# Kernel tuning notes

Hardware: AMD Instinct MI355X
Metric: run time of the kernel (lower is better)

Reference implementation:

```python
import jax, jax.numpy as jnp
import numpy as np


def setup_inputs() -> dict:
    key = jax.random.key(0)
    k1, k2 = jax.random.split(key)
    n_nodes, n_feat, n_edges = 100000, 64, 1600000
    x = jax.random.normal(k1, (n_nodes, n_feat), dtype=jnp.float32)
    edge_index = jax.random.randint(k2, (2, n_edges), 0, n_nodes, dtype=jnp.int64)
    return {"x": x, "edge_index": edge_index}


def reference(x, edge_index):
    # Faithful JAX version of OneHopGCNNormNodeLabelAggregator.forward:
    #   adj = SparseTensor.from_edge_index(edge_index)  (values = 1)
    #   adj_norm = gcn_norm(adj)  -> add self-loops (diag=1), symmetric D^-1/2 A D^-1/2
    #   x_neighbors = adj_norm.t() @ x
    n = x.shape[0]
    self_loops = jnp.arange(n, dtype=edge_index.dtype)
    row = jnp.concatenate([edge_index[0], self_loops])  # source of adj entry A[row, col]
    col = jnp.concatenate([edge_index[1], self_loops])
    # degree over rows (sparsesum dim=1 after fill_diag)
    deg = jax.ops.segment_sum(jnp.ones(row.shape, x.dtype), row, num_segments=n)
    deg_inv_sqrt = jnp.where(deg > 0, jax.lax.rsqrt(deg), 0.0).astype(x.dtype)
    # symmetric norm weight per edge
    w = deg_inv_sqrt[row] * deg_inv_sqrt[col]  # [E+n]
    # adj_norm.t() @ x : out[col] += w * x[row]
    x_neighbors = jax.ops.segment_sum(w[:, None] * x[row], col, num_segments=n)
    return x_neighbors
```

## Files before the change

kernel.cpp:

```cpp
#include <hip/hip_runtime.h>

#define NFEAT 64
#define BSHIFT 8
#define BCOLS 256
#define NBMAX 512
#define CAP 5120
#define CHUNK 3136
#define NITP 7
#define TPB 512
#define FBIT (CAP / TPB)
#define QCAP 1664


__device__ __forceinline__ unsigned short f2bf(float f) {
    unsigned int u = __float_as_uint(f);
    return (unsigned short)((u + 0x7FFFu + ((u >> 16) & 1u)) >> 16);
}
__device__ __forceinline__ float bflo(unsigned int u) {
    return __uint_as_float(u << 16);
}
__device__ __forceinline__ float bfhi(unsigned int u) {
    return __uint_as_float(u & 0xFFFF0000u);
}

__device__ __forceinline__ int wave_incl_scan(int v, int lane) {
    #pragma unroll
    for (int off = 1; off < 64; off <<= 1) {
        int u = __shfl_up(v, off);
        if (lane >= off) v += u;
    }
    return v;
}

__global__ __launch_bounds__(TPB)
void k_partCR(const int* __restrict__ rows, const int* __restrict__ cols,
              int* __restrict__ bcur, int* __restrict__ bcurR,
              int* __restrict__ part, unsigned char* __restrict__ partR, int E) {
    __shared__ int histC[NBMAX];
    __shared__ int histR[NBMAX];
    __shared__ int gbaseC[NBMAX];
    __shared__ int gbaseR[NBMAX];
    __shared__ int wsumC[8];
    __shared__ int wsumR[8];
    __shared__ int stageC[CHUNK];
    __shared__ unsigned char stageR[CHUNK];
    __shared__ unsigned short bidC[CHUNK];
    __shared__ unsigned short bidR[CHUNK];
    int chunk0 = blockIdx.x * CHUNK;
    int cnt = min(CHUNK, E - chunk0);
    int t = threadIdx.x;
    int lane = t & 63, wid = t >> 6;

    histC[t] = 0; histR[t] = 0;
    __syncthreads();

    int pk[NITP];
    unsigned char rpk[NITP];
    unsigned short cb[NITP], rb[NITP];
    unsigned short rkC[NITP], rkR[NITP];
    #pragma unroll
    for (int k = 0; k < NITP; k++) {
        int i = t + k * TPB;
        if (i < cnt) {
            int c = cols[chunk0 + i];
            int r = rows[chunk0 + i];
            int b  = c >> BSHIFT;
            int b2 = r >> BSHIFT;
            pk[k]  = ((c & (BCOLS - 1)) << 17) | r;
            rpk[k] = (unsigned char)(r & (BCOLS - 1));
            cb[k] = (unsigned short)b;
            rb[k] = (unsigned short)b2;
            rkC[k] = (unsigned short)atomicAdd(&histC[b], 1);
            rkR[k] = (unsigned short)atomicAdd(&histR[b2], 1);
        }
    }
    __syncthreads();

    int v1 = histC[t];
    int inc1 = wave_incl_scan(v1, lane);
    if (lane == 63) wsumC[wid] = inc1;
    int v2 = histR[t];
    int inc2 = wave_incl_scan(v2, lane);
    if (lane == 63) wsumR[wid] = inc2;
    __syncthreads();
    int addC = 0, addR = 0;
    #pragma unroll
    for (int k = 0; k < 8; k++) {
        if (k < wid) { addC += wsumC[k]; addR += wsumR[k]; }
    }
    int exC = inc1 - v1 + addC;
    int exR = inc2 - v2 + addR;
    gbaseC[t] = (v1 > 0) ? (t * CAP + atomicAdd(&bcur[t],  v1) - exC) : 0;
    gbaseR[t] = (v2 > 0) ? (t * CAP + atomicAdd(&bcurR[t], v2) - exR) : 0;
    histC[t] = exC;
    histR[t] = exR;
    __syncthreads();

    #pragma unroll
    for (int k = 0; k < NITP; k++) {
        int i = t + k * TPB;
        if (i < cnt) {
            int p = histC[cb[k]] + rkC[k];
            stageC[p] = pk[k];
            bidC[p] = cb[k];
            int p2 = histR[rb[k]] + rkR[k];
            stageR[p2] = rpk[k];
            bidR[p2] = rb[k];
        }
    }
    __syncthreads();

    for (int p = t; p < cnt; p += TPB) {
        int b = bidC[p];
        int idx = gbaseC[b] + p;
        if (idx < (b + 1) * CAP) part[idx] = stageC[p];
        int b2 = bidR[p];
        int idx2 = gbaseR[b2] + p;
        if (idx2 < (b2 + 1) * CAP) partR[idx2] = stageR[p];
    }
}

__global__ __launch_bounds__(TPB)
void k_fillR(const unsigned char* __restrict__ partR, const int* __restrict__ bcurR,
             const float4* __restrict__ x4, float* __restrict__ dinv,
             unsigned short* __restrict__ xs, int n) {
    __shared__ int lcnt[64];
    __shared__ float ldinv[64];
    int qb = blockIdx.x;
    int b = qb >> 2, q = qb & 3;
    int s = b * CAP;
    int t = threadIdx.x;
    int cntR = min(bcurR[b], CAP);
    if (t < 64) lcnt[t] = 0;
    __syncthreads();
    int c4 = cntR >> 2;
    const uchar4* p4 = (const uchar4*)(partR + s);
    for (int i = t; i < c4; i += TPB) {
        uchar4 kk = p4[i];
        if ((kk.x >> 6) == q) atomicAdd(&lcnt[kk.x & 63], 1);
        if ((kk.y >> 6) == q) atomicAdd(&lcnt[kk.y & 63], 1);
        if ((kk.z >> 6) == q) atomicAdd(&lcnt[kk.z & 63], 1);
        if ((kk.w >> 6) == q) atomicAdd(&lcnt[kk.w & 63], 1);
    }
    for (int i = (c4 << 2) + t; i < cntR; i += TPB) {
        int key = partR[s + i];
        if ((key >> 6) == q) atomicAdd(&lcnt[key & 63], 1);
    }
    __syncthreads();
    int rows_base = (b << BSHIFT) + (q << 6);
    if (t < 64) {
        float d = rsqrtf((float)(lcnt[t] + 1));
        ldinv[t] = d;
        int gr = rows_base + t;
        if (gr < n) dinv[gr] = d;
    }
    __syncthreads();
    int nr = n - rows_base;
    if (nr <= 0) return;
    size_t base4 = (size_t)rows_base << 4;
    int lim = min(64, nr) << 4;
    for (int i = t; i < lim; i += TPB) {
        float dd = ldinv[i >> 4];
        float4 vv = x4[base4 + i];
        ushort4 o;
        o.x = f2bf(dd * vv.x); o.y = f2bf(dd * vv.y);
        o.z = f2bf(dd * vv.z); o.w = f2bf(dd * vv.w);
        ((ushort4*)xs)[base4 + i] = o;
    }
}

#define XSLD(r) (*((const uint4*)(xs + ((size_t)(r) << 6)) + li))
#define ACC8(u) { a0 += bflo(u.x); a1 += bfhi(u.x); \
                  a2 += bflo(u.y); a3 += bfhi(u.y); \
                  a4 += bflo(u.z); a5 += bfhi(u.z); \
                  a6 += bflo(u.w); a7 += bfhi(u.w); }

__global__ __launch_bounds__(TPB)
void k_fuse(const int* __restrict__ part, const int* __restrict__ bcur,
            const unsigned short* __restrict__ xs,
            const float* __restrict__ dinv,
            float4* __restrict__ out4, int n) {
    __shared__ int lcnt[64];
    __shared__ int lps[64];
    __shared__ int stage[QCAP];
    int qb = blockIdx.x;
    int b = qb >> 2, q = qb & 3;
    int s = b * CAP;
    int cnt = min(bcur[b], CAP);
    int t = threadIdx.x;

    if (t < 64) lcnt[t] = 0;
    __syncthreads();

    int pk[FBIT];
    short rk[FBIT];
    #pragma unroll
    for (int k = 0; k < FBIT; k++) {
        int i = t + k * TPB;
        int v2 = (i < cnt) ? part[s + i] : -1;
        pk[k] = v2;
        rk[k] = -1;
        if (v2 >= 0) {
            int c = v2 >> 17;
            if ((c >> 6) == q)
                rk[k] = (short)atomicAdd(&lcnt[c & 63], 1);
        }
    }
    __syncthreads();

    if (t < 64) {
        int v = lcnt[t];
        int inc = wave_incl_scan(v, t);
        lps[t] = inc - v;
    }
    __syncthreads();

    #pragma unroll
    for (int k = 0; k < FBIT; k++) {
        if (rk[k] >= 0) {
            int c = (pk[k] >> 17) & 63;
            int p = lps[c] + rk[k];
            if (p < QCAP) stage[p] = pk[k] & 0x1FFFF;
        }
    }
    __syncthreads();

    int g = t >> 3, li = t & 7;
    int node = (b << BSHIFT) + (q << 6) + g;
    if (node >= n) return;
    int ss = lps[g];
    int len = lcnt[g];
    if (ss + len > QCAP) len = QCAP > ss ? QCAP - ss : 0;
    float a0 = 0.f, a1 = 0.f, a2 = 0.f, a3 = 0.f;
    float a4 = 0.f, a5 = 0.f, a6 = 0.f, a7 = 0.f;
    int len4 = len & ~3;
    uint4 c0, c1, c2, c3;
    if (len4 > 0) {
        int r0 = stage[ss], r1 = stage[ss + 1];
        int r2 = stage[ss + 2], r3 = stage[ss + 3];
        c0 = XSLD(r0); c1 = XSLD(r1); c2 = XSLD(r2); c3 = XSLD(r3);
    }
    for (int i = 4; i < len4; i += 4) {
        int r0 = stage[ss + i],     r1 = stage[ss + i + 1];
        int r2 = stage[ss + i + 2], r3 = stage[ss + i + 3];
        uint4 n0 = XSLD(r0), n1 = XSLD(r1), n2 = XSLD(r2), n3 = XSLD(r3);
        ACC8(c0); ACC8(c1); ACC8(c2); ACC8(c3);
        c0 = n0; c1 = n1; c2 = n2; c3 = n3;
    }
    if (len4 > 0) { ACC8(c0); ACC8(c1); ACC8(c2); ACC8(c3); }
    for (int i = len4; i < len; i++) {
        int r = stage[ss + i];
        uint4 u = XSLD(r);
        ACC8(u);
    }
    float dc = dinv[node];
    uint4 us = XSLD(node);
    float4 r0o, r1o;
    r0o.x = dc * (a0 + bflo(us.x));
    r0o.y = dc * (a1 + bfhi(us.x));
    r0o.z = dc * (a2 + bflo(us.y));
    r0o.w = dc * (a3 + bfhi(us.y));
    r1o.x = dc * (a4 + bflo(us.z));
    r1o.y = dc * (a5 + bfhi(us.z));
    r1o.z = dc * (a6 + bflo(us.w));
    r1o.w = dc * (a7 + bfhi(us.w));
    size_t ob = ((size_t)node << 4) + (li << 1);
    out4[ob] = r0o;
    out4[ob + 1] = r1o;
}

extern "C" void kernel_launch(void* const* d_in, const int* in_sizes, int n_in,
                              void* d_out, int out_size, void* d_ws, size_t ws_size,
                              hipStream_t stream) {
    const float* x    = (const float*)d_in[0];
    const int*   eidx = (const int*)d_in[1];

    int n = in_sizes[0] / NFEAT;
    int E = in_sizes[1] / 2;
    const int* rows = eidx;
    const int* cols = eidx + E;
    float* out = (float*)d_out;

    int nbuck = (n + BCOLS - 1) >> BSHIFT;

    char* w = (char*)d_ws;
    int*   bcur  = (int*)w;     w += NBMAX * 4;
    int*   bcurR = (int*)w;     w += NBMAX * 4;
    float* dinv  = (float*)w;   w += (size_t)n * 4;
    w = (char*)(((uintptr_t)w + 15) & ~(uintptr_t)15);
    unsigned short* xs = (unsigned short*)w;  w += (size_t)n * NFEAT * 2;
    int*   part  = (int*)w;     w += (size_t)nbuck * CAP * 4;
    unsigned char* partR = (unsigned char*)w;

    hipMemsetAsync(bcur, 0, NBMAX * 2 * 4, stream);

    int nchunk = (E + CHUNK - 1) / CHUNK;
    k_partCR<<<nchunk, TPB, 0, stream>>>(rows, cols, bcur, bcurR,
                                         part, partR, E);
    k_fillR<<<nbuck * 4, TPB, 0, stream>>>(partR, bcurR, (const float4*)x,
                                           dinv, xs, n);
    k_fuse<<<nbuck * 4, TPB, 0, stream>>>(part, bcur, xs, dinv,
                                          (float4*)out, n);
}
```

Before: 143.0 us.

## Process whole 256-column bucket per block instead of four quarter blocks

k_fillR and k_fuse now launch one block per bucket rather than four quarter-blocks, so each bucket's partition data is read and histogrammed once instead of four times. k_fuse stages all bucket edges into a CAP-sized shared buffer using a multi-wave scan, and loops over four 64-node groups per block. This cuts redundant reads of the partition data and redundant atomics, at the cost of a quarter as many blocks (about 391) and more shared memory per block, which lowers parallelism and occupancy.

```diff
diff --git a/kernel.cpp b/kernel.cpp
--- a/kernel.cpp
+++ b/kernel.cpp
@@ -9,7 +9,6 @@
 #define NITP 7
 #define TPB 512
 #define FBIT (CAP / TPB)
-#define QCAP 1664
 
 
 __device__ __forceinline__ unsigned short f2bf(float f) {
@@ -124,31 +123,28 @@
 void k_fillR(const unsigned char* __restrict__ partR, const int* __restrict__ bcurR,
              const float4* __restrict__ x4, float* __restrict__ dinv,
              unsigned short* __restrict__ xs, int n) {
-    __shared__ int lcnt[64];
-    __shared__ float ldinv[64];
-    int qb = blockIdx.x;
-    int b = qb >> 2, q = qb & 3;
+    __shared__ int lcnt[BCOLS];
+    __shared__ float ldinv[BCOLS];
+    int b = blockIdx.x;
     int s = b * CAP;
     int t = threadIdx.x;
     int cntR = min(bcurR[b], CAP);
-    if (t < 64) lcnt[t] = 0;
+    if (t < BCOLS) lcnt[t] = 0;
     __syncthreads();
     int c4 = cntR >> 2;
     const uchar4* p4 = (const uchar4*)(partR + s);
     for (int i = t; i < c4; i += TPB) {
         uchar4 kk = p4[i];
-        if ((kk.x >> 6) == q) atomicAdd(&lcnt[kk.x & 63], 1);
-        if ((kk.y >> 6) == q) atomicAdd(&lcnt[kk.y & 63], 1);
-        if ((kk.z >> 6) == q) atomicAdd(&lcnt[kk.z & 63], 1);
-        if ((kk.w >> 6) == q) atomicAdd(&lcnt[kk.w & 63], 1);
-    }
-    for (int i = (c4 << 2) + t; i < cntR; i += TPB) {
-        int key = partR[s + i];
-        if ((key >> 6) == q) atomicAdd(&lcnt[key & 63], 1);
-    }
-    __syncthreads();
-    int rows_base = (b << BSHIFT) + (q << 6);
-    if (t < 64) {
+        atomicAdd(&lcnt[kk.x], 1);
+        atomicAdd(&lcnt[kk.y], 1);
+        atomicAdd(&lcnt[kk.z], 1);
+        atomicAdd(&lcnt[kk.w], 1);
+    }
+    for (int i = (c4 << 2) + t; i < cntR; i += TPB)
+        atomicAdd(&lcnt[partR[s + i]], 1);
+    __syncthreads();
+    int rows_base = b << BSHIFT;
+    if (t < BCOLS) {
         float d = rsqrtf((float)(lcnt[t] + 1));
         ldinv[t] = d;
         int gr = rows_base + t;
@@ -158,7 +154,7 @@
     int nr = n - rows_base;
     if (nr <= 0) return;
     size_t base4 = (size_t)rows_base << 4;
-    int lim = min(64, nr) << 4;
+    int lim = min(BCOLS, nr) << 4;
     for (int i = t; i < lim; i += TPB) {
         float dd = ldinv[i >> 4];
         float4 vv = x4[base4 + i];
@@ -180,16 +176,17 @@
             const unsigned short* __restrict__ xs,
             const float* __restrict__ dinv,
             float4* __restrict__ out4, int n) {
-    __shared__ int lcnt[64];
-    __shared__ int lps[64];
-    __shared__ int stage[QCAP];
-    int qb = blockIdx.x;
-    int b = qb >> 2, q = qb & 3;
+    __shared__ int lcnt[BCOLS];
+    __shared__ int lps[BCOLS];
+    __shared__ int wsum[4];
+    __shared__ int stage[CAP];
+    int b = blockIdx.x;
     int s = b * CAP;
     int cnt = min(bcur[b], CAP);
     int t = threadIdx.x;
-
-    if (t < 64) lcnt[t] = 0;
+    int lane = t & 63, wid = t >> 6;
+
+    if (t < BCOLS) lcnt[t] = 0;
     __syncthreads();
 
     int pk[FBIT];
@@ -200,73 +197,83 @@
         int v2 = (i < cnt) ? part[s + i] : -1;
         pk[k] = v2;
         rk[k] = -1;
-        if (v2 >= 0) {
-            int c = v2 >> 17;
-            if ((c >> 6) == q)
-                rk[k] = (short)atomicAdd(&lcnt[c & 63], 1);
-        }
-    }
-    __syncthreads();
-
-    if (t < 64) {
-        int v = lcnt[t];
-        int inc = wave_incl_scan(v, t);
-        lps[t] = inc - v;
+        if (v2 >= 0)
+            rk[k] = (short)atomicAdd(&lcnt[v2 >> 17], 1);
+    }
+    __syncthreads();
+
+    int v = 0, inc = 0;
+    if (t < BCOLS) {
+        v = lcnt[t];
+        inc = wave_incl_scan(v, lane);
+        if (lane == 63) wsum[wid] = inc;
+    }
+    __syncthreads();
+    if (t < BCOLS) {
+        int add = 0;
+        if (wid > 0) add += wsum[0];
+        if (wid > 1) add += wsum[1];
+        if (wid > 2) add += wsum[2];
+        lps[t] = inc - v + add;
     }
     __syncthreads();
 
     #pragma unroll
     for (int k = 0; k < FBIT; k++) {
         if (rk[k] >= 0) {
-            int c = (pk[k] >> 17) & 63;
-            int p = lps[c] + rk[k];
-            if (p < QCAP) stage[p] = pk[k] & 0x1FFFF;
+            int v2 = pk[k];
+            stage[lps[v2 >> 17] + rk[k]] = v2 & 0x1FFFF;
         }
     }
     __syncthreads();
 
-    int g = t >> 3, li = t & 7;
-    int node = (b << BSHIFT) + (q << 6) + g;
-    if (node >= n) return;
-    int ss = lps[g];
-    int len = lcnt[g];
-    if (ss + len > QCAP) len = QCAP > ss ? QCAP - ss : 0;
-    float a0 = 0.f, a1 = 0.f, a2 = 0.f, a3 = 0.f;
-    float a4 = 0.f, a5 = 0.f, a6 = 0.f, a7 = 0.f;
-    int len4 = len & ~3;
-    uint4 c0, c1, c2, c3;
-    if (len4 > 0) {
-        int r0 = stage[ss], r1 = stage[ss + 1];
-        int r2 = stage[ss + 2], r3 = stage[ss + 3];
-        c0 = XSLD(r0); c1 = XSLD(r1); c2 = XSLD(r2); c3 = XSLD(r3);
-    }
-    for (int i = 4; i < len4; i += 4) {
-        int r0 = stage[ss + i],     r1 = stage[ss + i + 1];
-        int r2 = stage[ss + i + 2], r3 = stage[ss + i + 3];
-        uint4 n0 = XSLD(r0), n1 = XSLD(r1), n2 = XSLD(r2), n3 = XSLD(r3);
-        ACC8(c0); ACC8(c1); ACC8(c2); ACC8(c3);
-        c0 = n0; c1 = n1; c2 = n2; c3 = n3;
-    }
-    if (len4 > 0) { ACC8(c0); ACC8(c1); ACC8(c2); ACC8(c3); }
-    for (int i = len4; i < len; i++) {
-        int r = stage[ss + i];
-        uint4 u = XSLD(r);
-        ACC8(u);
-    }
-    float dc = dinv[node];
-    uint4 us = XSLD(node);
-    float4 r0o, r1o;
-    r0o.x = dc * (a0 + bflo(us.x));
-    r0o.y = dc * (a1 + bfhi(us.x));
-    r0o.z = dc * (a2 + bflo(us.y));
-    r0o.w = dc * (a3 + bfhi(us.y));
-    r1o.x = dc * (a4 + bflo(us.z));
-    r1o.y = dc * (a5 + bfhi(us.z));
-    r1o.z = dc * (a6 + bflo(us.w));
-    r1o.w = dc * (a7 + bfhi(us.w));
-    size_t ob = ((size_t)node << 4) + (li << 1);
-    out4[ob] = r0o;
-    out4[ob + 1] = r1o;
+    int gg = t >> 3, li = t & 7;
+    #pragma unroll
+    for (int cc = 0; cc < BCOLS; cc += 64) {
+        int c = cc + gg;
+        int node = (b << BSHIFT) + c;
+        if (node < n) {
+            int ss = lps[c];
+            int len = lcnt[c];
+            float a0 = 0.f, a1 = 0.f, a2 = 0.f, a3 = 0.f;
+            float a4 = 0.f, a5 = 0.f, a6 = 0.f, a7 = 0.f;
+            int len4 = len & ~3;
+            uint4 c0, c1, c2, c3;
+            if (len4 > 0) {
+                int r0 = stage[ss], r1 = stage[ss + 1];
+                int r2 = stage[ss + 2], r3 = stage[ss + 3];
+                c0 = XSLD(r0); c1 = XSLD(r1); c2 = XSLD(r2); c3 = XSLD(r3);
+            }
+            for (int i = 4; i < len4; i += 4) {
+                int r0 = stage[ss + i],     r1 = stage[ss + i + 1];
+                int r2 = stage[ss + i + 2], r3 = stage[ss + i + 3];
+                uint4 n0 = XSLD(r0), n1 = XSLD(r1);
+                uint4 n2 = XSLD(r2), n3 = XSLD(r3);
+                ACC8(c0); ACC8(c1); ACC8(c2); ACC8(c3);
+                c0 = n0; c1 = n1; c2 = n2; c3 = n3;
+            }
+            if (len4 > 0) { ACC8(c0); ACC8(c1); ACC8(c2); ACC8(c3); }
+            for (int i = len4; i < len; i++) {
+                int r = stage[ss + i];
+                uint4 u = XSLD(r);
+                ACC8(u);
+            }
+            float dc = dinv[node];
+            uint4 us = XSLD(node);
+            float4 r0o, r1o;
+            r0o.x = dc * (a0 + bflo(us.x));
+            r0o.y = dc * (a1 + bfhi(us.x));
+            r0o.z = dc * (a2 + bflo(us.y));
+            r0o.w = dc * (a3 + bfhi(us.y));
+            r1o.x = dc * (a4 + bflo(us.z));
+            r1o.y = dc * (a5 + bfhi(us.z));
+            r1o.z = dc * (a6 + bflo(us.w));
+            r1o.w = dc * (a7 + bfhi(us.w));
+            size_t ob = ((size_t)node << 4) + (li << 1);
+            out4[ob] = r0o;
+            out4[ob + 1] = r1o;
+        }
+    }
 }
 
 extern "C" void kernel_launch(void* const* d_in, const int* in_sizes, int n_in,
@@ -297,8 +304,8 @@
     int nchunk = (E + CHUNK - 1) / CHUNK;
     k_partCR<<<nchunk, TPB, 0, stream>>>(rows, cols, bcur, bcurR,
                                          part, partR, E);
-    k_fillR<<<nbuck * 4, TPB, 0, stream>>>(partR, bcurR, (const float4*)x,
-                                           dinv, xs, n);
-    k_fuse<<<nbuck * 4, TPB, 0, stream>>>(part, bcur, xs, dinv,
-                                          (float4*)out, n);
-}
+    k_fillR<<<nbuck, TPB, 0, stream>>>(partR, bcurR, (const float4*)x,
+                                       dinv, xs, n);
+    k_fuse<<<nbuck, TPB, 0, stream>>>(part, bcur, xs, dinv,
+                                      (float4*)out, n);
+}
```

Result: no change. 142.6 us (-0.3%).
